# Kernel optimization log

Measured on AMD Instinct MI355X. Metric: run time of the kernel, lower is better.

Reference implementation:

```python
import jax, jax.numpy as jnp
import numpy as np

N = 50000      # nodes
E = 600000     # edges
IN = 128       # in_channels
C = 32         # hidden_channels
H = 4          # heads
L = 3          # num_layers
NEG_SLOPE = 0.2


def setup_inputs() -> dict:
    key = jax.random.key(0)
    ks = jax.random.split(key, 2 + 6 * L)
    d = {
        "x": jax.random.normal(ks[0], (N, IN), jnp.float32),
        "edge_index": jax.random.randint(ks[1], (2, E), 0, N, dtype=jnp.int64),
    }
    dims_in = [IN, H * C, H * C]
    s = 0.1
    for l in range(L):
        kk = ks[2 + 6 * l: 2 + 6 * (l + 1)]
        out_dim = H * C if l < L - 1 else C
        d[f"W{l}"] = jax.random.normal(kk[0], (dims_in[l], H * C), jnp.float32) * s
        d[f"linb{l}"] = jnp.zeros((H * C,), jnp.float32)
        d[f"att{l}"] = jax.random.normal(kk[1], (H, C), jnp.float32) * s
        d[f"bias{l}"] = jnp.zeros((out_dim,), jnp.float32)
        d[f"skipW{l}"] = jax.random.normal(kk[2], (dims_in[l], out_dim), jnp.float32) * s
        d[f"skipb{l}"] = jnp.zeros((out_dim,), jnp.float32)
    return d


def _gatv2_layer(x, src, dst, W, linb, att, bias, concat):
    # share_weights=True and x_target == x  ->  single projection for src & dst
    n = x.shape[0]
    h = (x @ W + linb).reshape(n, H, C)                      # [N,H,C]
    e = jax.nn.leaky_relu(h[src] + h[dst], NEG_SLOPE)        # [E,H,C]
    score = jnp.einsum('ehc,hc->eh', e, att)                 # [E,H]
    # scatter-softmax over incoming edges of each destination node
    m = jax.ops.segment_max(score, dst, num_segments=n)      # [N,H]
    p = jnp.exp(score - m[dst])                              # [E,H]
    denom = jax.ops.segment_sum(p, dst, num_segments=n)      # [N,H]
    alpha = p / jnp.maximum(denom[dst], 1e-16)               # [E,H]
    out = jax.ops.segment_sum(alpha[:, :, None] * h[src], dst, num_segments=n)  # [N,H,C]
    out = out.reshape(n, H * C) if concat else out.mean(axis=1)
    return out + bias


def reference(x, edge_index,
              W0, linb0, att0, bias0, skipW0, skipb0,
              W1, linb1, att1, bias1, skipW1, skipb1,
              W2, linb2, att2, bias2, skipW2, skipb2):
    src, dst = edge_index[0], edge_index[1]
    params = [
        (W0, linb0, att0, bias0, skipW0, skipb0),
        (W1, linb1, att1, bias1, skipW1, skipb1),
        (W2, linb2, att2, bias2, skipW2, skipb2),
    ]
    for l, (W, linb, att, bias, sW, sb) in enumerate(params):
        out = _gatv2_layer(x, src, dst, W, linb, att, bias, concat=(l < L - 1))
        x = out + (x @ sW + sb)                              # skip connection
        if l != L - 1:
            x = jax.nn.elu(x)                                # dropout is identity in eval mode
    return x
```

## Files before the change

kernel.cpp:

```cpp
#include <hip/hip_runtime.h>
#include <hip/hip_bf16.h>

#define NN 50000
#define NE 600000
#define IN_DIM 128
#define HC 128
#define NH 4
#define NC 32
#define NEG_SLOPE 0.2f

#define NTHR 256
#define NTILE 196
#define WT_TOTAL 86016
#define NG32 1563
#define GHIST 2344
#define XCONV 800000
#define NGAT16 3125

typedef __attribute__((ext_vector_type(8))) short short8;
typedef __attribute__((ext_vector_type(4))) float floatx4;
typedef __attribute__((ext_vector_type(8))) unsigned short ushort8v;

__device__ __forceinline__ float bf2f(unsigned short u) {
    return __uint_as_float(((unsigned)u) << 16);
}
__device__ __forceinline__ unsigned short f2bf(float f) {
    unsigned u = __float_as_uint(f);
    unsigned r = (u + 0x7FFFu + ((u >> 16) & 1u)) >> 16;
    return (unsigned short)r;
}

template<int OD, int NTC, int PIT>
__device__ __forceinline__ void gemm_wave_compute(
    const unsigned short* __restrict__ x, const unsigned short* __restrict__ Wt,
    const float* __restrict__ b, unsigned short (* __restrict__ tile)[PIT],
    int n0, int c016, int lane) {
    int quad = lane >> 4, l16 = lane & 15;
    floatx4 acc[2][NTC];
    #pragma unroll
    for (int i = 0; i < 2; ++i)
        #pragma unroll
        for (int j = 0; j < NTC; ++j) acc[i][j] = (floatx4){0.f, 0.f, 0.f, 0.f};

    int r0 = n0 + l16;      if (r0 >= NN) r0 = NN - 1;
    int r1 = n0 + 16 + l16; if (r1 >= NN) r1 = NN - 1;
    int lidx = (quad * 16 + l16) * 8;

    #pragma unroll
    for (int ks = 0; ks < 4; ++ks) {
        int kb = ks * 32 + quad * 8;
        short8 xb0 = *(const short8*)&x[(size_t)r0 * IN_DIM + kb];
        short8 xb1 = *(const short8*)&x[(size_t)r1 * IN_DIM + kb];
        #pragma unroll
        for (int tc = 0; tc < NTC; ++tc) {
            int grp = ks * (OD / 16) + c016 + tc;
            short8 af = *(const short8*)&Wt[grp * 512 + lidx];
            acc[0][tc] = __builtin_amdgcn_mfma_f32_16x16x32_bf16(af, xb0, acc[0][tc], 0, 0, 0);
            acc[1][tc] = __builtin_amdgcn_mfma_f32_16x16x32_bf16(af, xb1, acc[1][tc], 0, 0, 0);
        }
    }

    #pragma unroll
    for (int tc = 0; tc < NTC; ++tc) {
        int cbase = (c016 + tc) * 16 + quad * 4;
        float4 bv = *(const float4*)&b[cbase];
        #pragma unroll
        for (int i = 0; i < 2; ++i) {
            ushort4 pk = {f2bf(acc[i][tc][0] + bv.x), f2bf(acc[i][tc][1] + bv.y),
                          f2bf(acc[i][tc][2] + bv.z), f2bf(acc[i][tc][3] + bv.w)};
            *(ushort4*)&tile[i * 16 + l16][cbase] = pk;
        }
    }
}

__device__ __forceinline__ void store_tile128(
    const unsigned short (* __restrict__ tile)[136],
    unsigned short* __restrict__ y, int n0, int pt) {
    #pragma unroll
    for (int s = 0; s < 4; ++s) {
        int idx = s * 128 + pt;
        int node = idx >> 4, t16 = idx & 15;
        if (n0 + node < NN)
            *(ushort8v*)&y[(size_t)(n0 + node) * 128 + t16 * 8] =
                *(const ushort8v*)&tile[node][t16 * 8];
    }
}

__global__ __launch_bounds__(256) void k_gat(
    const unsigned short* __restrict__ h, const int* __restrict__ rowptr,
    const int* __restrict__ csr_src, const float* __restrict__ att,
    const float* __restrict__ bias, const unsigned short* __restrict__ skip,
    void* __restrict__ out, int last) {
    int lane = threadIdx.x & 63;
    int wid = threadIdx.x >> 6;
    int slot = lane >> 4, t = lane & 15;
    int lbase = slot << 4;

    int nv = blockIdx.x * 16 + wid * 4 + slot;
    bool valid = nv < NN;
    int n = valid ? nv : NN - 1;

    ushort8v skv = 0;
    if (!last)       skv = *(const ushort8v*)(skip + (size_t)n * HC + t * 8);
    else if (t < 4)  skv = *(const ushort8v*)(skip + (size_t)n * NC + t * 8);

    int beg = rowptr[n], end = rowptr[n + 1];
    int deg = end - beg;

    int idv = 0;
    if (t < deg) idv = csr_src[beg + t];

    ushort8v hdv = *(const ushort8v*)(h + (size_t)n * HC + t * 8);
    float hd[8], av[8];
    #pragma unroll
    for (int c = 0; c < 8; ++c) hd[c] = bf2f(hdv[c]);
    float4 av0 = ((const float4*)att)[t * 2];
    float4 av1 = ((const float4*)att)[t * 2 + 1];
    av[0] = av0.x; av[1] = av0.y; av[2] = av0.z; av[3] = av0.w;
    av[4] = av1.x; av[5] = av1.y; av[6] = av1.z; av[7] = av1.w;

    float K = 0.f;
    #pragma unroll
    for (int c = 0; c < 8; ++c) K = fmaf(hd[c], av[c], K);

    const unsigned short* hp = h + t * 8;

    int id0 = __shfl(idv, lbase + 0, 64);
    int id1 = __shfl(idv, lbase + 1, 64);
    int id2 = __shfl(idv, lbase + 2, 64);
    int id3 = __shfl(idv, lbase + 3, 64);
    ushort8v g0 = 0, g1 = 0, g2 = 0, g3 = 0;
    if (deg > 0) g0 = *(const ushort8v*)(hp + id0);
    if (deg > 1) g1 = *(const ushort8v*)(hp + id1);
    if (deg > 2) g2 = *(const ushort8v*)(hp + id2);
    if (deg > 3) g3 = *(const ushort8v*)(hp + id3);

    float l = 0.f;
    float acc[8] = {};

    auto gstep = [&](ushort8v& G, int k) {
        float hs[8];
        float S1 = K, S2 = 0.f;
        #pragma unroll
        for (int c = 0; c < 8; ++c) {
            float hsv = bf2f(G[c]);
            hs[c] = hsv;
            S1 = fmaf(hsv, av[c], S1);
            S2 = fmaf(fabsf(hsv + hd[c]), av[c], S2);
        }
        int kn = k + 4;
        if (kn < deg) {
            int idn = (kn < 16) ? __shfl(idv, lbase + kn, 64) : csr_src[beg + kn];
            G = *(const ushort8v*)(hp + idn);
        }
        float part = fmaf(0.6f, S1, 0.4f * S2);
        part += __shfl_xor(part, 1, 64);
        part += __shfl_xor(part, 2, 64);
        float p = __expf(part);
        #pragma unroll
        for (int c = 0; c < 8; ++c) acc[c] = fmaf(p, hs[c], acc[c]);
        l += p;
    };

    int k = 0;
    if (deg > 0) for (;;) {
        gstep(g0, k); if (++k >= deg) break;
        gstep(g1, k); if (++k >= deg) break;
        gstep(g2, k); if (++k >= deg) break;
        gstep(g3, k); if (++k >= deg) break;
    }

    float inv = 1.f / fmaxf(l, 1e-16f);
    float o[8];
    #pragma unroll
    for (int c = 0; c < 8; ++c) o[c] = acc[c] * inv;

    if (!last) {
        float4 bv0 = ((const float4*)bias)[t * 2];
        float4 bv1 = ((const float4*)bias)[t * 2 + 1];
        float bb[8] = {bv0.x, bv0.y, bv0.z, bv0.w, bv1.x, bv1.y, bv1.z, bv1.w};
        ushort8v ov;
        #pragma unroll
        for (int c = 0; c < 8; ++c) {
            float r = o[c] + bb[c] + bf2f(skv[c]);
            r = r > 0.f ? r : (__expf(r) - 1.f);
            ov[c] = f2bf(r);
        }
        if (valid)
            *(ushort8v*)((unsigned short*)out + (size_t)n * HC + t * 8) = ov;
    } else {
        float r4[8], r8[8], r12[8];
        #pragma unroll
        for (int c = 0; c < 8; ++c) {
            r4[c]  = __shfl_down(o[c], 4, 16);
            r8[c]  = __shfl_down(o[c], 8, 16);
            r12[c] = __shfl_down(o[c], 12, 16);
        }
        if (t < 4 && valid) {
            float* op = (float*)out + (size_t)n * NC + t * 8;
            float rr[8];
            #pragma unroll
            for (int c = 0; c < 8; ++c) {
                rr[c] = 0.25f * (o[c] + r4[c] + r8[c] + r12[c])
                      + bias[t * 8 + c] + bf2f(skv[c]);
            }
            *(float4*)op = (float4){rr[0], rr[1], rr[2], rr[3]};
            *(float4*)(op + 4) = (float4){rr[4], rr[5], rr[6], rr[7]};
        }
    }
}


__global__ void k_prep(const float* __restrict__ W0, const float* __restrict__ S0,
                       const float* __restrict__ W1, const float* __restrict__ S1,
                       const float* __restrict__ W2, const float* __restrict__ S2,
                       const float* __restrict__ x0, unsigned short* __restrict__ xbuf,
                       unsigned short* __restrict__ wt, int* __restrict__ deg) {
    int idx = blockIdx.x * blockDim.x + threadIdx.x;
    if (idx < WT_TOTAL) {
        if (idx < 81920) {
            int r = idx >> 14;
            const float* W = (r == 0) ? W0 : (r == 1) ? S0 : (r == 2) ? W1 : (r == 3) ? S1 : W2;
            int off = idx & 16383;
            int j = off & 7, l16 = (off >> 3) & 15, quad = (off >> 7) & 3;
            int cg = (off >> 9) & 7, ks = off >> 12;
            int k = ks * 32 + quad * 8 + j;
            int col = cg * 16 + l16;
            wt[idx] = f2bf(W[(size_t)k * 128 + col]);
        } else {
            int off = idx - 81920;
            int j = off & 7, l16 = (off >> 3) & 15, quad = (off >> 7) & 3;
            int cg = (off >> 9) & 1, ks = off >> 10;
            int k = ks * 32 + quad * 8 + j;
            int col = cg * 16 + l16;
            wt[idx] = f2bf(S2[(size_t)k * 32 + col]);
        }
        return;
    }
    int i = idx - WT_TOTAL;
    if (i < NN) { deg[i] = 0; return; }
    int j = i - NN;
    if (j < XCONV) {
        const float* xp = x0 + (size_t)j * 8;
        float4 a = *(const float4*)xp;
        float4 b = *(const float4*)(xp + 4);
        ushort8v v;
        v[0] = f2bf(a.x); v[1] = f2bf(a.y); v[2] = f2bf(a.z); v[3] = f2bf(a.w);
        v[4] = f2bf(b.x); v[5] = f2bf(b.y); v[6] = f2bf(b.z); v[7] = f2bf(b.w);
        *(ushort8v*)(xbuf + (size_t)j * 8) = v;
    }
}

__global__ __launch_bounds__(256) void k_gemm0_hist(
    const unsigned short* __restrict__ x,
    const unsigned short* __restrict__ Wta, const float* __restrict__ ba, unsigned short* __restrict__ ya,
    const unsigned short* __restrict__ Wtb, const float* __restrict__ bb, unsigned short* __restrict__ yb,
    const int* __restrict__ dst, int* __restrict__ deg) {
    __shared__ unsigned short tA[32][136];
    __shared__ unsigned short tB[32][136];
    int b = blockIdx.x;
    if (b < NG32) {
        int wid = threadIdx.x >> 6, lane = threadIdx.x & 63;
        int n0 = b * 32;
        if (wid < 2) gemm_wave_compute<128, 4, 136>(x, Wta, ba, tA, n0, wid * 4, lane);
        else         gemm_wave_compute<128, 4, 136>(x, Wtb, bb, tB, n0, (wid - 2) * 4, lane);
        __syncthreads();
        int pt = threadIdx.x & 127;
        if (threadIdx.x < 128) store_tile128(tA, ya, n0, pt);
        else                   store_tile128(tB, yb, n0, pt);
    } else {
        int e = (b - NG32) * 256 + threadIdx.x;
        if (e < NE) atomicAdd(&deg[dst[e]], 1);
    }
}

__global__ __launch_bounds__(NTHR) void k_scan1(const int* __restrict__ deg,
                                                int* __restrict__ partial,
                                                int* __restrict__ blocksum) {
    __shared__ int sh[NTHR];
    int b = blockIdx.x, t = threadIdx.x;
    int i = b * NTHR + t;
    int d = (i < NN) ? deg[i] : 0;
    sh[t] = d;
    __syncthreads();
    #pragma unroll
    for (int off = 1; off < NTHR; off <<= 1) {
        int v = (t >= off) ? sh[t - off] : 0;
        __syncthreads();
        sh[t] += v;
        __syncthreads();
    }
    if (i < NN) partial[i] = sh[t];
    if (t == NTHR - 1) blocksum[b] = sh[t];
}

__global__ __launch_bounds__(NTHR) void k_scan23(const int* __restrict__ deg,
                                                 const int* __restrict__ partial,
                                                 const int* __restrict__ blocksum,
                                                 int* __restrict__ rowptr,
                                                 int* __restrict__ cursor) {
    __shared__ int sh[NTHR];
    int b = blockIdx.x, t = threadIdx.x;
    int v = (t < NTILE) ? blocksum[t] : 0;
    sh[t] = v;
    __syncthreads();
    #pragma unroll
    for (int off = 1; off < NTHR; off <<= 1) {
        int u = (t >= off) ? sh[t - off] : 0;
        __syncthreads();
        sh[t] += u;
        __syncthreads();
    }
    int tile_off = (b > 0) ? sh[b - 1] : 0;
    int i = b * NTHR + t;
    if (i < NN) {
        int inc = partial[i] + tile_off;
        rowptr[i + 1] = inc;
        cursor[i] = inc - deg[i];
        if (i == 0) rowptr[0] = 0;
    }
}

__global__ void k_scatter(const int* __restrict__ src, const int* __restrict__ dst,
                          int* __restrict__ cursor, int* __restrict__ csr_src) {
    int e = blockIdx.x * blockDim.x + threadIdx.x;
    if (e >= NE) return;
    int d = dst[e];
    int pos = atomicAdd(&cursor[d], 1);
    csr_src[pos] = src[e] * HC;
}

__global__ __launch_bounds__(256) void k_gemm_dual(
    const unsigned short* __restrict__ x,
    const unsigned short* __restrict__ Wta, const float* __restrict__ ba, unsigned short* __restrict__ ya,
    const unsigned short* __restrict__ Wtb, const float* __restrict__ bb, unsigned short* __restrict__ yb) {
    __shared__ unsigned short tA[32][136];
    __shared__ unsigned short tB[32][136];
    int wid = threadIdx.x >> 6, lane = threadIdx.x & 63;
    int n0 = blockIdx.x * 32;
    if (wid < 2) gemm_wave_compute<128, 4, 136>(x, Wta, ba, tA, n0, wid * 4, lane);
    else         gemm_wave_compute<128, 4, 136>(x, Wtb, bb, tB, n0, (wid - 2) * 4, lane);
    __syncthreads();
    int pt = threadIdx.x & 127;
    if (threadIdx.x < 128) store_tile128(tA, ya, n0, pt);
    else                   store_tile128(tB, yb, n0, pt);
}

__global__ __launch_bounds__(256) void k_gemm_dual_l2(
    const unsigned short* __restrict__ x,
    const unsigned short* __restrict__ Wta, const float* __restrict__ ba, unsigned short* __restrict__ ya,
    const unsigned short* __restrict__ Wtb, const float* __restrict__ bb, unsigned short* __restrict__ yb) {
    __shared__ unsigned short tA[32][136];
    __shared__ unsigned short tB[32][40];
    int wid = threadIdx.x >> 6, lane = threadIdx.x & 63;
    int n0 = blockIdx.x * 32;
    if (wid < 2) gemm_wave_compute<128, 4, 136>(x, Wta, ba, tA, n0, wid * 4, lane);
    else         gemm_wave_compute<32, 1, 40>(x, Wtb, bb, tB, n0, wid - 2, lane);
    __syncthreads();
    if (threadIdx.x < 128) {
        store_tile128(tA, ya, n0, threadIdx.x);
    } else {
        int pt = threadIdx.x - 128;
        int node = pt >> 2, t4 = pt & 3;
        if (n0 + node < NN)
            *(ushort8v*)&yb[(size_t)(n0 + node) * 32 + t4 * 8] =
                *(const ushort8v*)&tB[node][t4 * 8];
    }
}

extern "C" void kernel_launch(void* const* d_in, const int* in_sizes, int n_in,
                              void* d_out, int out_size, void* d_ws, size_t ws_size,
                              hipStream_t stream) {
    const float* x0 = (const float*)d_in[0];
    const int* ei = (const int*)d_in[1];
    const int* src = ei;
    const int* dst = ei + NE;

    unsigned short* xbuf = (unsigned short*)d_ws;
    unsigned short* h    = xbuf + (size_t)NN * HC;
    unsigned short* skip = h + (size_t)NN * HC;
    int* deg     = (int*)(skip + (size_t)NN * HC);
    int* rowptr  = deg + NN;
    int* cursor  = rowptr + NN + 1;
    int* partial = cursor + NN;
    int* blocksum = partial + NN;
    uintptr_t pa = (uintptr_t)(blocksum + NTILE);
    pa = (pa + 15) & ~(uintptr_t)15;
    unsigned short* wt = (unsigned short*)pa;
    int* csr_src = (int*)(wt + WT_TOTAL);

    unsigned short* wtW[3] = {wt, wt + 32768, wt + 65536};
    unsigned short* wtS[3] = {wt + 16384, wt + 49152, wt + 81920};

    const float* linb0  = (const float*)d_in[3];
    const float* skipb0 = (const float*)d_in[7];

    k_prep<<<(WT_TOTAL + NN + XCONV + 255) / 256, 256, 0, stream>>>(
        (const float*)d_in[2], (const float*)d_in[6],
        (const float*)d_in[8], (const float*)d_in[12],
        (const float*)d_in[14], (const float*)d_in[18],
        x0, xbuf, wt, deg);

    k_gemm0_hist<<<NG32 + GHIST, 256, 0, stream>>>(
        xbuf, wtW[0], linb0, h, wtS[0], skipb0, skip, dst, deg);

    k_scan1<<<NTILE, NTHR, 0, stream>>>(deg, partial, blocksum);
    k_scan23<<<NTILE, NTHR, 0, stream>>>(deg, partial, blocksum, rowptr, cursor);
    k_scatter<<<GHIST, 256, 0, stream>>>(src, dst, cursor, csr_src);

    for (int l = 0; l < 3; ++l) {
        const float* linb  = (const float*)d_in[2 + 6 * l + 1];
        const float* att   = (const float*)d_in[2 + 6 * l + 2];
        const float* bias  = (const float*)d_in[2 + 6 * l + 3];
        const float* skipb = (const float*)d_in[2 + 6 * l + 5];

        if (l == 1) {
            k_gemm_dual<<<NG32, 256, 0, stream>>>(
                xbuf, wtW[1], linb, h, wtS[1], skipb, skip);
        } else if (l == 2) {
            k_gemm_dual_l2<<<NG32, 256, 0, stream>>>(
                xbuf, wtW[2], linb, h, wtS[2], skipb, skip);
        }
        void* outp = (l < 2) ? (void*)xbuf : (void*)d_out;
        k_gat<<<NGAT16, 256, 0, stream>>>(h, rowptr, csr_src, att, bias, skip, outp, l == 2);
    }
}
```

Measured before the change: 302.8 us.

## Fuse next-layer projection GEMMs into GAT aggregation kernels and drop input conversion pass

Each non-final GAT aggregation kernel now writes its ELU output for 16 nodes into LDS and immediately runs the next layer's h and skip projections with MFMA. This removes the separate GEMM launches and the global round trip of the intermediate activations. Layer 0's GEMM reads fp32 input directly and converts to bf16 in registers, so the prep kernel no longer does a separate conversion pass. Ping-pong H/S buffers avoid read-after-write hazards. In exchange, each block gains a barrier and LDS use, and GEMM tiles are smaller at 16 rows, so weight loads are reused less.

```diff
diff --git a/kernel.cpp b/kernel.cpp
--- a/kernel.cpp
+++ b/kernel.cpp
@@ -14,7 +14,6 @@
 #define WT_TOTAL 86016
 #define NG32 1563
 #define GHIST 2344
-#define XCONV 800000
 #define NGAT16 3125
 
 typedef __attribute__((ext_vector_type(8))) short short8;
@@ -30,9 +29,9 @@
     return (unsigned short)r;
 }
 
-template<int OD, int NTC, int PIT>
+template<typename AT, int OD, int NTC, int PIT>
 __device__ __forceinline__ void gemm_wave_compute(
-    const unsigned short* __restrict__ x, const unsigned short* __restrict__ Wt,
+    const AT* __restrict__ x, const unsigned short* __restrict__ Wt,
     const float* __restrict__ b, unsigned short (* __restrict__ tile)[PIT],
     int n0, int c016, int lane) {
     int quad = lane >> 4, l16 = lane & 15;
@@ -49,8 +48,21 @@
     #pragma unroll
     for (int ks = 0; ks < 4; ++ks) {
         int kb = ks * 32 + quad * 8;
-        short8 xb0 = *(const short8*)&x[(size_t)r0 * IN_DIM + kb];
-        short8 xb1 = *(const short8*)&x[(size_t)r1 * IN_DIM + kb];
+        short8 xb0, xb1;
+        if constexpr (sizeof(AT) == 4) {
+            const float* xr = (const float*)x;
+            float4 v0 = *(const float4*)&xr[(size_t)r0 * IN_DIM + kb];
+            float4 v1 = *(const float4*)&xr[(size_t)r0 * IN_DIM + kb + 4];
+            float4 u0 = *(const float4*)&xr[(size_t)r1 * IN_DIM + kb];
+            float4 u1 = *(const float4*)&xr[(size_t)r1 * IN_DIM + kb + 4];
+            xb0 = (short8){(short)f2bf(v0.x), (short)f2bf(v0.y), (short)f2bf(v0.z), (short)f2bf(v0.w),
+                           (short)f2bf(v1.x), (short)f2bf(v1.y), (short)f2bf(v1.z), (short)f2bf(v1.w)};
+            xb1 = (short8){(short)f2bf(u0.x), (short)f2bf(u0.y), (short)f2bf(u0.z), (short)f2bf(u0.w),
+                           (short)f2bf(u1.x), (short)f2bf(u1.y), (short)f2bf(u1.z), (short)f2bf(u1.w)};
+        } else {
+            xb0 = *(const short8*)&((const unsigned short*)x)[(size_t)r0 * IN_DIM + kb];
+            xb1 = *(const short8*)&((const unsigned short*)x)[(size_t)r1 * IN_DIM + kb];
+        }
         #pragma unroll
         for (int tc = 0; tc < NTC; ++tc) {
             int grp = ks * (OD / 16) + c016 + tc;
@@ -86,27 +98,65 @@
     }
 }
 
-__global__ __launch_bounds__(256) void k_gat(
+template<int OD, int NTC, int PITX, int PITO>
+__device__ __forceinline__ void gemm16_lds(
+    const unsigned short (* __restrict__ xt)[PITX], const unsigned short* __restrict__ Wt,
+    const float* __restrict__ b, unsigned short (* __restrict__ tile)[PITO],
+    int c016, int lane) {
+    int quad = lane >> 4, l16 = lane & 15;
+    floatx4 acc[NTC];
+    #pragma unroll
+    for (int j = 0; j < NTC; ++j) acc[j] = (floatx4){0.f, 0.f, 0.f, 0.f};
+    int lidx = (quad * 16 + l16) * 8;
+
+    #pragma unroll
+    for (int ks = 0; ks < 4; ++ks) {
+        int kb = ks * 32 + quad * 8;
+        short8 xb = *(const short8*)&xt[l16][kb];
+        #pragma unroll
+        for (int tc = 0; tc < NTC; ++tc) {
+            int grp = ks * (OD / 16) + c016 + tc;
+            short8 af = *(const short8*)&Wt[grp * 512 + lidx];
+            acc[tc] = __builtin_amdgcn_mfma_f32_16x16x32_bf16(af, xb, acc[tc], 0, 0, 0);
+        }
+    }
+
+    #pragma unroll
+    for (int tc = 0; tc < NTC; ++tc) {
+        int cbase = (c016 + tc) * 16 + quad * 4;
+        float4 bv = *(const float4*)&b[cbase];
+        ushort4 pk = {f2bf(acc[tc][0] + bv.x), f2bf(acc[tc][1] + bv.y),
+                      f2bf(acc[tc][2] + bv.z), f2bf(acc[tc][3] + bv.w)};
+        *(ushort4*)&tile[l16][cbase] = pk;
+    }
+}
+
+template<int SOD>
+__global__ __launch_bounds__(256) void k_gat_gemm(
     const unsigned short* __restrict__ h, const int* __restrict__ rowptr,
     const int* __restrict__ csr_src, const float* __restrict__ att,
-    const float* __restrict__ bias, const unsigned short* __restrict__ skip,
-    void* __restrict__ out, int last) {
+    const float* __restrict__ gbias, const unsigned short* __restrict__ gskip,
+    const unsigned short* __restrict__ WtA, const float* __restrict__ linb,
+    unsigned short* __restrict__ yh,
+    const unsigned short* __restrict__ WtB, const float* __restrict__ skipb,
+    unsigned short* __restrict__ yskip) {
+    __shared__ unsigned short xt[16][136];
+    __shared__ unsigned short th[16][136];
+    __shared__ unsigned short ts[16][136];
+
     int lane = threadIdx.x & 63;
     int wid = threadIdx.x >> 6;
     int slot = lane >> 4, t = lane & 15;
     int lbase = slot << 4;
-
-    int nv = blockIdx.x * 16 + wid * 4 + slot;
+    int nloc = wid * 4 + slot;
+    int nv = blockIdx.x * 16 + nloc;
     bool valid = nv < NN;
     int n = valid ? nv : NN - 1;
 
-    ushort8v skv = 0;
-    if (!last)       skv = *(const ushort8v*)(skip + (size_t)n * HC + t * 8);
-    else if (t < 4)  skv = *(const ushort8v*)(skip + (size_t)n * NC + t * 8);
+    ushort8v skv = *(const ushort8v*)(gskip + (size_t)n * HC + t * 8);
 
     int beg = rowptr[n], end = rowptr[n + 1];
     int deg = end - beg;
-
     int idv = 0;
     if (t < deg) idv = csr_src[beg + t];
 
@@ -124,7 +174,6 @@
     for (int c = 0; c < 8; ++c) K = fmaf(hd[c], av[c], K);
 
     const unsigned short* hp = h + t * 8;
-
     int id0 = __shfl(idv, lbase + 0, 64);
     int id1 = __shfl(idv, lbase + 1, 64);
     int id2 = __shfl(idv, lbase + 2, 64);
@@ -171,42 +220,151 @@
     }
 
     float inv = 1.f / fmaxf(l, 1e-16f);
+    float4 bv0 = ((const float4*)gbias)[t * 2];
+    float4 bv1 = ((const float4*)gbias)[t * 2 + 1];
+    float bb[8] = {bv0.x, bv0.y, bv0.z, bv0.w, bv1.x, bv1.y, bv1.z, bv1.w};
+    ushort8v ov;
+    #pragma unroll
+    for (int c = 0; c < 8; ++c) {
+        float r = acc[c] * inv + bb[c] + bf2f(skv[c]);
+        r = r > 0.f ? r : (__expf(r) - 1.f);
+        ov[c] = f2bf(r);
+    }
+    *(ushort8v*)&xt[nloc][t * 8] = ov;
+
+    __syncthreads();
+
+    if (wid < 2)           gemm16_lds<128, 4, 136, 136>(xt, WtA, linb, th, wid * 4, lane);
+    else if (SOD == 128)   gemm16_lds<128, 4, 136, 136>(xt, WtB, skipb, ts, (wid - 2) * 4, lane);
+    else                   gemm16_lds<32, 1, 136, 136>(xt, WtB, skipb, ts, wid - 2, lane);
+
+    __syncthreads();
+
+    int p = threadIdx.x;
+    {
+        int node = p >> 4, t16 = p & 15;
+        int gn = blockIdx.x * 16 + node;
+        if (gn < NN)
+            *(ushort8v*)&yh[(size_t)gn * 128 + t16 * 8] = *(const ushort8v*)&th[node][t16 * 8];
+    }
+    if (SOD == 128) {
+        int node = p >> 4, t16 = p & 15;
+        int gn = blockIdx.x * 16 + node;
+        if (gn < NN)
+            *(ushort8v*)&yskip[(size_t)gn * 128 + t16 * 8] = *(const ushort8v*)&ts[node][t16 * 8];
+    } else {
+        if (p < 64) {
+            int node = p >> 2, t4 = p & 3;
+            int gn = blockIdx.x * 16 + node;
+            if (gn < NN)
+                *(ushort8v*)&yskip[(size_t)gn * 32 + t4 * 8] = *(const ushort8v*)&ts[node][t4 * 8];
+        }
+    }
+}
+
+__global__ __launch_bounds__(256) void k_gat_last(
+    const unsigned short* __restrict__ h, const int* __restrict__ rowptr,
+    const int* __restrict__ csr_src, const float* __restrict__ att,
+    const float* __restrict__ bias, const unsigned short* __restrict__ skip,
+    float* __restrict__ out) {
+    int lane = threadIdx.x & 63;
+    int wid = threadIdx.x >> 6;
+    int slot = lane >> 4, t = lane & 15;
+    int lbase = slot << 4;
+
+    int nv = blockIdx.x * 16 + wid * 4 + slot;
+    bool valid = nv < NN;
+    int n = valid ? nv : NN - 1;
+
+    ushort8v skv = 0;
+    if (t < 4) skv = *(const ushort8v*)(skip + (size_t)n * NC + t * 8);
+
+    int beg = rowptr[n], end = rowptr[n + 1];
+    int deg = end - beg;
+    int idv = 0;
+    if (t < deg) idv = csr_src[beg + t];
+
+    ushort8v hdv = *(const ushort8v*)(h + (size_t)n * HC + t * 8);
+    float hd[8], av[8];
+    #pragma unroll
+    for (int c = 0; c < 8; ++c) hd[c] = bf2f(hdv[c]);
+    float4 av0 = ((const float4*)att)[t * 2];
+    float4 av1 = ((const float4*)att)[t * 2 + 1];
+    av[0] = av0.x; av[1] = av0.y; av[2] = av0.z; av[3] = av0.w;
+    av[4] = av1.x; av[5] = av1.y; av[6] = av1.z; av[7] = av1.w;
+
+    float K = 0.f;
+    #pragma unroll
+    for (int c = 0; c < 8; ++c) K = fmaf(hd[c], av[c], K);
+
+    const unsigned short* hp = h + t * 8;
+    int id0 = __shfl(idv, lbase + 0, 64);
+    int id1 = __shfl(idv, lbase + 1, 64);
+    int id2 = __shfl(idv, lbase + 2, 64);
+    int id3 = __shfl(idv, lbase + 3, 64);
+    ushort8v g0 = 0, g1 = 0, g2 = 0, g3 = 0;
+    if (deg > 0) g0 = *(const ushort8v*)(hp + id0);
+    if (deg > 1) g1 = *(const ushort8v*)(hp + id1);
+    if (deg > 2) g2 = *(const ushort8v*)(hp + id2);
+    if (deg > 3) g3 = *(const ushort8v*)(hp + id3);
+
+    float l = 0.f;
+    float acc[8] = {};
+
+    auto gstep = [&](ushort8v& G, int k) {
+        float hs[8];
+        float S1 = K, S2 = 0.f;
+        #pragma unroll
+        for (int c = 0; c < 8; ++c) {
+            float hsv = bf2f(G[c]);
+            hs[c] = hsv;
+            S1 = fmaf(hsv, av[c], S1);
+            S2 = fmaf(fabsf(hsv + hd[c]), av[c], S2);
+        }
+        int kn = k + 4;
+        if (kn < deg) {
+            int idn = (kn < 16) ? __shfl(idv, lbase + kn, 64) : csr_src[beg + kn];
+            G = *(const ushort8v*)(hp + idn);
+        }
+        float part = fmaf(0.6f, S1, 0.4f * S2);
+        part += __shfl_xor(part, 1, 64);
+        part += __shfl_xor(part, 2, 64);
+        float p = __expf(part);
+        #pragma unroll
+        for (int c = 0; c < 8; ++c) acc[c] = fmaf(p, hs[c], acc[c]);
+        l += p;
+    };
+
+    int k = 0;
+    if (deg > 0) for (;;) {
+        gstep(g0, k); if (++k >= deg) break;
+        gstep(g1, k); if (++k >= deg) break;
+        gstep(g2, k); if (++k >= deg) break;
+        gstep(g3, k); if (++k >= deg) break;
+    }
+
+    float inv = 1.f / fmaxf(l, 1e-16f);
     float o[8];
     #pragma unroll
     for (int c = 0; c < 8; ++c) o[c] = acc[c] * inv;
 
-    if (!last) {
-        float4 bv0 = ((const float4*)bias)[t * 2];
-        float4 bv1 = ((const float4*)bias)[t * 2 + 1];
-        float bb[8] = {bv0.x, bv0.y, bv0.z, bv0.w, bv1.x, bv1.y, bv1.z, bv1.w};
-        ushort8v ov;
+    float r4[8], r8[8], r12[8];
+    #pragma unroll
+    for (int c = 0; c < 8; ++c) {
+        r4[c]  = __shfl_down(o[c], 4, 16);
+        r8[c]  = __shfl_down(o[c], 8, 16);
+        r12[c] = __shfl_down(o[c], 12, 16);
+    }
+    if (t < 4 && valid) {
+        float* op = out + (size_t)n * NC + t * 8;
+        float rr[8];
         #pragma unroll
         for (int c = 0; c < 8; ++c) {
-            float r = o[c] + bb[c] + bf2f(skv[c]);
-            r = r > 0.f ? r : (__expf(r) - 1.f);
-            ov[c] = f2bf(r);
-        }
-        if (valid)
-            *(ushort8v*)((unsigned short*)out + (size_t)n * HC + t * 8) = ov;
-    } else {
-        float r4[8], r8[8], r12[8];
-        #pragma unroll
-        for (int c = 0; c < 8; ++c) {
-            r4[c]  = __shfl_down(o[c], 4, 16);
-            r8[c]  = __shfl_down(o[c], 8, 16);
-            r12[c] = __shfl_down(o[c], 12, 16);
-        }
-        if (t < 4 && valid) {
-            float* op = (float*)out + (size_t)n * NC + t * 8;
-            float rr[8];
-            #pragma unroll
-            for (int c = 0; c < 8; ++c) {
-                rr[c] = 0.25f * (o[c] + r4[c] + r8[c] + r12[c])
-                      + bias[t * 8 + c] + bf2f(skv[c]);
-            }
-            *(float4*)op = (float4){rr[0], rr[1], rr[2], rr[3]};
-            *(float4*)(op + 4) = (float4){rr[4], rr[5], rr[6], rr[7]};
-        }
+            rr[c] = 0.25f * (o[c] + r4[c] + r8[c] + r12[c])
+                  + bias[t * 8 + c] + bf2f(skv[c]);
+        }
+        *(float4*)op = (float4){rr[0], rr[1], rr[2], rr[3]};
+        *(float4*)(op + 4) = (float4){rr[4], rr[5], rr[6], rr[7]};
     }
 }
 
@@ -214,7 +372,6 @@
 __global__ void k_prep(const float* __restrict__ W0, const float* __restrict__ S0,
                        const float* __restrict__ W1, const float* __restrict__ S1,
                        const float* __restrict__ W2, const float* __restrict__ S2,
-                       const float* __restrict__ x0, unsigned short* __restrict__ xbuf,
                        unsigned short* __restrict__ wt, int* __restrict__ deg) {
     int idx = blockIdx.x * blockDim.x + threadIdx.x;
     if (idx < WT_TOTAL) {
@@ -238,21 +395,11 @@
         return;
     }
     int i = idx - WT_TOTAL;
-    if (i < NN) { deg[i] = 0; return; }
-    int j = i - NN;
-    if (j < XCONV) {
-        const float* xp = x0 + (size_t)j * 8;
-        float4 a = *(const float4*)xp;
-        float4 b = *(const float4*)(xp + 4);
-        ushort8v v;
-        v[0] = f2bf(a.x); v[1] = f2bf(a.y); v[2] = f2bf(a.z); v[3] = f2bf(a.w);
-        v[4] = f2bf(b.x); v[5] = f2bf(b.y); v[6] = f2bf(b.z); v[7] = f2bf(b.w);
-        *(ushort8v*)(xbuf + (size_t)j * 8) = v;
-    }
+    if (i < NN) deg[i] = 0;
 }
 
 __global__ __launch_bounds__(256) void k_gemm0_hist(
-    const unsigned short* __restrict__ x,
+    const float* __restrict__ x,
     const unsigned short* __restrict__ Wta, const float* __restrict__ ba, unsigned short* __restrict__ ya,
     const unsigned short* __restrict__ Wtb, const float* __restrict__ bb, unsigned short* __restrict__ yb,
     const int* __restrict__ dst, int* __restrict__ deg) {
@@ -262,8 +409,8 @@
     if (b < NG32) {
         int wid = threadIdx.x >> 6, lane = threadIdx.x & 63;
         int n0 = b * 32;
-        if (wid < 2) gemm_wave_compute<128, 4, 136>(x, Wta, ba, tA, n0, wid * 4, lane);
-        else         gemm_wave_compute<128, 4, 136>(x, Wtb, bb, tB, n0, (wid - 2) * 4, lane);
+        if (wid < 2) gemm_wave_compute<float, 128, 4, 136>(x, Wta, ba, tA, n0, wid * 4, lane);
+        else         gemm_wave_compute<float, 128, 4, 136>(x, Wtb, bb, tB, n0, (wid - 2) * 4, lane);
         __syncthreads();
         int pt = threadIdx.x & 127;
         if (threadIdx.x < 128) store_tile128(tA, ya, n0, pt);
@@ -330,44 +477,6 @@
     csr_src[pos] = src[e] * HC;
 }
 
-__global__ __launch_bounds__(256) void k_gemm_dual(
-    const unsigned short* __restrict__ x,
-    const unsigned short* __restrict__ Wta, const float* __restrict__ ba, unsigned short* __restrict__ ya,
-    const unsigned short* __restrict__ Wtb, const float* __restrict__ bb, unsigned short* __restrict__ yb) {
-    __shared__ unsigned short tA[32][136];
-    __shared__ unsigned short tB[32][136];
-    int wid = threadIdx.x >> 6, lane = threadIdx.x & 63;
-    int n0 = blockIdx.x * 32;
-    if (wid < 2) gemm_wave_compute<128, 4, 136>(x, Wta, ba, tA, n0, wid * 4, lane);
-    else         gemm_wave_compute<128, 4, 136>(x, Wtb, bb, tB, n0, (wid - 2) * 4, lane);
-    __syncthreads();
-    int pt = threadIdx.x & 127;
-    if (threadIdx.x < 128) store_tile128(tA, ya, n0, pt);
-    else                   store_tile128(tB, yb, n0, pt);
-}
-
-__global__ __launch_bounds__(256) void k_gemm_dual_l2(
-    const unsigned short* __restrict__ x,
-    const unsigned short* __restrict__ Wta, const float* __restrict__ ba, unsigned short* __restrict__ ya,
-    const unsigned short* __restrict__ Wtb, const float* __restrict__ bb, unsigned short* __restrict__ yb) {
-    __shared__ unsigned short tA[32][136];
-    __shared__ unsigned short tB[32][40];
-    int wid = threadIdx.x >> 6, lane = threadIdx.x & 63;
-    int n0 = blockIdx.x * 32;
-    if (wid < 2) gemm_wave_compute<128, 4, 136>(x, Wta, ba, tA, n0, wid * 4, lane);
-    else         gemm_wave_compute<32, 1, 40>(x, Wtb, bb, tB, n0, wid - 2, lane);
-    __syncthreads();
-    if (threadIdx.x < 128) {
-        store_tile128(tA, ya, n0, threadIdx.x);
-    } else {
-        int pt = threadIdx.x - 128;
-        int node = pt >> 2, t4 = pt & 3;
-        if (n0 + node < NN)
-            *(ushort8v*)&yb[(size_t)(n0 + node) * 32 + t4 * 8] =
-                *(const ushort8v*)&tB[node][t4 * 8];
-    }
-}
-
 extern "C" void kernel_launch(void* const* d_in, const int* in_sizes, int n_in,
                               void* d_out, int out_size, void* d_ws, size_t ws_size,
                               hipStream_t stream) {
@@ -376,10 +485,11 @@
     const int* src = ei;
     const int* dst = ei + NE;
 
-    unsigned short* xbuf = (unsigned short*)d_ws;
-    unsigned short* h    = xbuf + (size_t)NN * HC;
-    unsigned short* skip = h + (size_t)NN * HC;
-    int* deg     = (int*)(skip + (size_t)NN * HC);
+    unsigned short* H0 = (unsigned short*)d_ws;
+    unsigned short* S0 = H0 + (size_t)NN * HC;
+    unsigned short* H1 = S0 + (size_t)NN * HC;
+    unsigned short* S1 = H1 + (size_t)NN * HC;
+    int* deg     = (int*)(S1 + (size_t)NN * HC);
     int* rowptr  = deg + NN;
     int* cursor  = rowptr + NN + 1;
     int* partial = cursor + NN;
@@ -392,36 +502,32 @@
     unsigned short* wtW[3] = {wt, wt + 32768, wt + 65536};
     unsigned short* wtS[3] = {wt + 16384, wt + 49152, wt + 81920};
 
-    const float* linb0  = (const float*)d_in[3];
-    const float* skipb0 = (const float*)d_in[7];
-
-    k_prep<<<(WT_TOTAL + NN + XCONV + 255) / 256, 256, 0, stream>>>(
+    k_prep<<<(WT_TOTAL + NN + 255) / 256, 256, 0, stream>>>(
         (const float*)d_in[2], (const float*)d_in[6],
         (const float*)d_in[8], (const float*)d_in[12],
-        (const float*)d_in[14], (const float*)d_in[18],
-        x0, xbuf, wt, deg);
+        (const float*)d_in[14], (const float*)d_in[18], wt, deg);
 
     k_gemm0_hist<<<NG32 + GHIST, 256, 0, stream>>>(
-        xbuf, wtW[0], linb0, h, wtS[0], skipb0, skip, dst, deg);
+        x0, wtW[0], (const float*)d_in[3], H0,
+        wtS[0], (const float*)d_in[7], S0, dst, deg);
 
     k_scan1<<<NTILE, NTHR, 0, stream>>>(deg, partial, blocksum);
     k_scan23<<<NTILE, NTHR, 0, stream>>>(deg, partial, blocksum, rowptr, cursor);
     k_scatter<<<GHIST, 256, 0, stream>>>(src, dst, cursor, csr_src);
 
-    for (int l = 0; l < 3; ++l) {
-        const float* linb  = (const float*)d_in[2 + 6 * l + 1];
-        const float* att   = (const float*)d_in[2 + 6 * l + 2];
-        const float* bias  = (const float*)d_in[2 + 6 * l + 3];
-        const float* skipb = (const float*)d_in[2 + 6 * l + 5];
-
-        if (l == 1) {
-            k_gemm_dual<<<NG32, 256, 0, stream>>>(
-                xbuf, wtW[1], linb, h, wtS[1], skipb, skip);
-        } else if (l == 2) {
-            k_gemm_dual_l2<<<NG32, 256, 0, stream>>>(
-                xbuf, wtW[2], linb, h, wtS[2], skipb, skip);
-        }
-        void* outp = (l < 2) ? (void*)xbuf : (void*)d_out;
-        k_gat<<<NGAT16, 256, 0, stream>>>(h, rowptr, csr_src, att, bias, skip, outp, l == 2);
-    }
-}
+    k_gat_gemm<128><<<NGAT16, 256, 0, stream>>>(
+        H0, rowptr, csr_src,
+        (const float*)d_in[4], (const float*)d_in[5], S0,
+        wtW[1], (const float*)d_in[9], H1,
+        wtS[1], (const float*)d_in[13], S1);
+
+    k_gat_gemm<32><<<NGAT16, 256, 0, stream>>>(
+        H1, rowptr, csr_src,
+        (const float*)d_in[10], (const float*)d_in[11], S1,
+        wtW[2], (const float*)d_in[15], H0,
+        wtS[2], (const float*)d_in[19], S0);
+
+    k_gat_last<<<NGAT16, 256, 0, stream>>>(
+        H0, rowptr, csr_src,
+        (const float*)d_in[16], (const float*)d_in[17], S0, (float*)d_out);
+}
```

Result: faster. 284.8 us (-6.0%).
